# Kernel optimization log

Hardware: AMD Instinct MI355X
Metric: run time of the kernel (lower is better)

## Reference

```python
import jax, jax.numpy as jnp
import numpy as np

NUM_HEADS = 16
THRESHOLD = 4e-4  # < 1/S so every softmax row keeps >=1 entry (classical path of grover_search_filter)


def setup_inputs() -> dict:
    key = jax.random.key(0)
    k0, k1, k2 = jax.random.split(key, 3)
    B, S, E = 4, 1024, 1024
    x = jax.random.normal(k0, (B, S, E), dtype=jnp.float32)
    Wqkv = jax.random.normal(k1, (3 * E, E), dtype=jnp.float32) * 0.02
    bqkv = jnp.zeros((3 * E,), dtype=jnp.float32)
    Wproj = jax.random.normal(k2, (E, E), dtype=jnp.float32) * 0.02
    bproj = jnp.zeros((E,), dtype=jnp.float32)
    return {"x": x, "Wqkv": Wqkv, "bqkv": bqkv, "Wproj": Wproj, "bproj": bproj}


def reference(x, Wqkv, bqkv, Wproj, bproj):
    B, S, E = x.shape
    H = NUM_HEADS
    D = E // H
    scale = D ** -0.5
    # qkv projection -> (3, B, H, S, D), matching torch permute(2,0,3,1,4)
    qkv = (x @ Wqkv.T + bqkv).reshape(B, S, 3, H, D).transpose(2, 0, 3, 1, 4)
    q, k, v = qkv[0], qkv[1], qkv[2]
    attn_logits = jnp.einsum("bhqd,bhkd->bhqk", q, k) * scale  # [B,H,S,S]
    attn_probs = jax.nn.softmax(attn_logits, axis=-1)
    # grover_search_filter: seq_len > 2**max_qubits -> classical threshold mask
    selected = attn_probs > THRESHOLD
    filtered_logits = jnp.where(selected, attn_logits, -jnp.inf)
    filtered_attn = jax.nn.softmax(filtered_logits, axis=-1)
    # dropout is identity in eval mode
    out = jnp.einsum("bhqk,bhkd->bhqd", filtered_attn, v)
    out = out.transpose(0, 2, 1, 3).reshape(B, S, E)
    out = out @ Wproj.T + bproj
    return out, filtered_attn
```

## Files before the change

kernel.cpp:

```cpp
#include <hip/hip_runtime.h>
#include <hip/hip_bf16.h>
#include <cstdint>


#define BB 4
#define SS 1024
#define EE 1024
#define HH 16
#define DD 64

typedef __attribute__((ext_vector_type(8))) short bf16x8;
typedef __attribute__((ext_vector_type(4))) float f32x4;

__global__ __launch_bounds__(256) void split_f32(
    const float* __restrict__ in, __hip_bfloat16* __restrict__ hi,
    __hip_bfloat16* __restrict__ lo, int n4) {
  int i = blockIdx.x * 256 + threadIdx.x;
  if (i >= n4) return;
  float4 v = ((const float4*)in)[i];
  float vv[4] = {v.x, v.y, v.z, v.w};
  __hip_bfloat16 h[4], l[4];
#pragma unroll
  for (int j = 0; j < 4; ++j) {
    h[j] = __float2bfloat16(vv[j]);
    l[j] = __float2bfloat16(vv[j] - __bfloat162float(h[j]));
  }
  ((ushort4*)hi)[i] = *(ushort4*)h;
  if (lo) ((ushort4*)lo)[i] = *(ushort4*)l;
}

template <int MODE>
__global__ __launch_bounds__(256) void gemm(
    const __hip_bfloat16* __restrict__ Ah, const __hip_bfloat16* __restrict__ Al,
    const __hip_bfloat16* __restrict__ Bh, const __hip_bfloat16* __restrict__ Bl,
    const float* __restrict__ Af, const float* __restrict__ bias,
    float* __restrict__ oF, __hip_bfloat16* __restrict__ o1,
    __hip_bfloat16* __restrict__ o2, __hip_bfloat16* __restrict__ o3,
    __hip_bfloat16* __restrict__ o4, __hip_bfloat16* __restrict__ o5,
    int M, int N, int K, int lda, int ldb, long long sA, long long sB) {
  constexpr bool SPLIT = (MODE == 0 || MODE == 1);
  constexpr bool AF32  = (MODE == 2);

  const int tid  = threadIdx.x;
  const int lane = tid & 63;
  const int wave = tid >> 6;
  const int wm   = (wave >> 1) * 64;
  const int wn   = (wave & 1) * 64;
  const int quad = lane >> 4;
  const int l15  = lane & 15;
  const int m0   = blockIdx.y * 128;
  const int n0   = blockIdx.x * 128;
  const long long zz = blockIdx.z;

  if (AF32) Af += zz * sA;
  else { Ah += zz * sA; if (SPLIT) Al += zz * sA; }
  Bh += zz * sB;
  if (SPLIT) Bl += zz * sB;

  __shared__ __align__(16) __hip_bfloat16 lds[(SPLIT ? 4 : 2) * 128 * 72];
  __hip_bfloat16* lAh = lds;
  __hip_bfloat16* lAl = SPLIT ? lds + 128 * 72 : nullptr;
  __hip_bfloat16* lBh = lds + (SPLIT ? 2 : 1) * 128 * 72;
  __hip_bfloat16* lBl = SPLIT ? lds + 3 * 128 * 72 : nullptr;

  f32x4 acc[4][4] = {};

  for (int k0 = 0; k0 < K; k0 += 64) {
#pragma unroll
    for (int it = 0; it < 4; ++it) {
      int flat = (it * 256 + tid) * 8;
      int row  = flat >> 6;
      int kk   = flat & 63;
      const bool mok = (m0 + row < M);
      const bool nok = (n0 + row < N);
      if (AF32) {
        float4 f0 = {0, 0, 0, 0}, f1 = {0, 0, 0, 0};
        if (mok) {
          const float* src = Af + (long long)(m0 + row) * lda + k0 + kk;
          f0 = *(const float4*)src;
          f1 = *(const float4*)(src + 4);
        }
        __hip_bfloat16 t[8];
        t[0] = __float2bfloat16(f0.x); t[1] = __float2bfloat16(f0.y);
        t[2] = __float2bfloat16(f0.z); t[3] = __float2bfloat16(f0.w);
        t[4] = __float2bfloat16(f1.x); t[5] = __float2bfloat16(f1.y);
        t[6] = __float2bfloat16(f1.z); t[7] = __float2bfloat16(f1.w);
        *(uint4*)&lAh[row * 72 + kk] = *(uint4*)t;
      } else {
        uint4 va = {0, 0, 0, 0};
        if (mok) va = *(const uint4*)(Ah + (long long)(m0 + row) * lda + k0 + kk);
        *(uint4*)&lAh[row * 72 + kk] = va;
        if (SPLIT) {
          uint4 vl = {0, 0, 0, 0};
          if (mok) vl = *(const uint4*)(Al + (long long)(m0 + row) * lda + k0 + kk);
          *(uint4*)&lAl[row * 72 + kk] = vl;
        }
      }
      uint4 vb = {0, 0, 0, 0};
      if (nok) vb = *(const uint4*)(Bh + (long long)(n0 + row) * ldb + k0 + kk);
      *(uint4*)&lBh[row * 72 + kk] = vb;
      if (SPLIT) {
        uint4 vbl = {0, 0, 0, 0};
        if (nok) vbl = *(const uint4*)(Bl + (long long)(n0 + row) * ldb + k0 + kk);
        *(uint4*)&lBl[row * 72 + kk] = vbl;
      }
    }
    __syncthreads();

#pragma unroll
    for (int ks = 0; ks < 64; ks += 32) {
      bf16x8 ah[4], bh[4], al[4], bl[4];
#pragma unroll
      for (int i = 0; i < 4; ++i) {
        int off = (wm + i * 16 + l15) * 72 + ks + quad * 8;
        ah[i] = *(const bf16x8*)&lAh[off];
        if (SPLIT) al[i] = *(const bf16x8*)&lAl[off];
      }
#pragma unroll
      for (int j = 0; j < 4; ++j) {
        int off = (wn + j * 16 + l15) * 72 + ks + quad * 8;
        bh[j] = *(const bf16x8*)&lBh[off];
        if (SPLIT) bl[j] = *(const bf16x8*)&lBl[off];
      }
#pragma unroll
      for (int i = 0; i < 4; ++i)
#pragma unroll
        for (int j = 0; j < 4; ++j) {
          if (SPLIT) {
            acc[i][j] = __builtin_amdgcn_mfma_f32_16x16x32_bf16(al[i], bh[j], acc[i][j], 0, 0, 0);
            acc[i][j] = __builtin_amdgcn_mfma_f32_16x16x32_bf16(ah[i], bl[j], acc[i][j], 0, 0, 0);
          }
          acc[i][j] = __builtin_amdgcn_mfma_f32_16x16x32_bf16(ah[i], bh[j], acc[i][j], 0, 0, 0);
        }
    }
    __syncthreads();
  }

#pragma unroll
  for (int i = 0; i < 4; ++i) {
#pragma unroll
    for (int j = 0; j < 4; ++j) {
#pragma unroll
      for (int r = 0; r < 4; ++r) {
        int m = m0 + wm + i * 16 + quad * 4 + r;
        int n = n0 + wn + j * 16 + l15;
        float v = acc[i][j][r];
        if (MODE == 0) {
          v += bias[n];
          int c = n >> 10, nn = n & 1023, h = nn >> 6, d = nn & 63;
          int b = m >> 10, s = m & 1023;
          long long idx = (((long long)(b * HH + h) * SS + s) << 6) + d;
          if (c == 0) {
            __hip_bfloat16 hh = __float2bfloat16(v);
            o1[idx] = hh;
            o2[idx] = __float2bfloat16(v - __bfloat162float(hh));
          } else if (c == 1) {
            __hip_bfloat16 hh = __float2bfloat16(v);
            o3[idx] = hh;
            o4[idx] = __float2bfloat16(v - __bfloat162float(hh));
          } else {
            o5[(((long long)(b * HH + h) * DD + d) << 10) + s] = __float2bfloat16(v);
          }
        } else if (MODE == 1) {
          oF[zz * (SS * SS) + (long long)m * SS + n] = v * 0.125f;
        } else if (MODE == 2) {
          if (n < DD) {
            int b = (int)(zz >> 4), h = (int)(zz & 15);
            o1[(((long long)(b * SS + m)) << 10) + h * DD + n] = __float2bfloat16(v);
          }
        } else {
          oF[(long long)m * EE + n] = v + bias[n];
        }
      }
    }
  }
}

__device__ __forceinline__ float qg_max16(float v) {
#pragma unroll
  for (int o = 8; o > 0; o >>= 1) v = fmaxf(v, __shfl_xor(v, o));
  return v;
}
__device__ __forceinline__ float qg_sum16(float v) {
#pragma unroll
  for (int o = 8; o > 0; o >>= 1) v += __shfl_xor(v, o);
  return v;
}

__global__ __launch_bounds__(256, 4) void fused_attn(
    const __hip_bfloat16* __restrict__ qh, const __hip_bfloat16* __restrict__ ql,
    const __hip_bfloat16* __restrict__ kh, const __hip_bfloat16* __restrict__ kl,
    const __hip_bfloat16* __restrict__ vT, float* __restrict__ attn,
    __hip_bfloat16* __restrict__ ao) {
  const int tid  = threadIdx.x;
  const int lane = tid & 63;
  const int wave = tid >> 6;
  const int quad = lane >> 4;
  const int l15  = lane & 15;

  int id = blockIdx.x;
  const int q8 = gridDim.x >> 3;
  id = (id & 7) * q8 + (id >> 3);
  const int bh = id >> 6;
  const int q0 = (id & 63) * 16;

  const int brow = (bh >> 4) * SS;
  const int h    = bh & 15;
  const long long qbase = ((long long)bh * SS + q0) * DD;
  const long long kbase = (long long)bh * SS * DD;
  const long long vbase = (long long)bh * DD * SS;
  const long long abase = ((long long)bh * SS + q0) * SS;

  __shared__ __align__(16) __hip_bfloat16 Pl[16][1032];
  __shared__ float red[3][4][16];

  bf16x8 aqh0, aqh1, aql0, aql1;
  {
    const __hip_bfloat16* ph = qh + qbase + l15 * DD + quad * 8;
    const __hip_bfloat16* pl = ql + qbase + l15 * DD + quad * 8;
    aqh0 = *(const bf16x8*)(ph);
    aqh1 = *(const bf16x8*)(ph + 32);
    aql0 = *(const bf16x8*)(pl);
    aql1 = *(const bf16x8*)(pl + 32);
  }

  f32x4 acc[16];
  const __hip_bfloat16* pkh0 = kh + kbase + (long long)(wave * 256 + l15) * DD + quad * 8;
  const __hip_bfloat16* pkl0 = kl + kbase + (long long)(wave * 256 + l15) * DD + quad * 8;
#pragma unroll
  for (int nt = 0; nt < 16; ++nt) {
    const __hip_bfloat16* pkh = pkh0 + nt * 16 * DD;
    const __hip_bfloat16* pkl = pkl0 + nt * 16 * DD;
    bf16x8 b0 = *(const bf16x8*)(pkh);
    bf16x8 b1 = *(const bf16x8*)(pkh + 32);
    bf16x8 c0 = *(const bf16x8*)(pkl);
    bf16x8 c1 = *(const bf16x8*)(pkl + 32);
    f32x4 a = {};
    a = __builtin_amdgcn_mfma_f32_16x16x32_bf16(aql0, b0, a, 0, 0, 0);
    a = __builtin_amdgcn_mfma_f32_16x16x32_bf16(aqh0, c0, a, 0, 0, 0);
    a = __builtin_amdgcn_mfma_f32_16x16x32_bf16(aqh0, b0, a, 0, 0, 0);
    a = __builtin_amdgcn_mfma_f32_16x16x32_bf16(aql1, b1, a, 0, 0, 0);
    a = __builtin_amdgcn_mfma_f32_16x16x32_bf16(aqh1, c1, a, 0, 0, 0);
    a = __builtin_amdgcn_mfma_f32_16x16x32_bf16(aqh1, b1, a, 0, 0, 0);
    acc[nt] = a;
  }

#pragma unroll
  for (int nt = 0; nt < 16; ++nt)
#pragma unroll
    for (int r = 0; r < 4; ++r) acc[nt][r] *= 0.125f;

  float mx[4];
#pragma unroll
  for (int r = 0; r < 4; ++r) {
    float mm = acc[0][r];
#pragma unroll
    for (int nt = 1; nt < 16; ++nt) mm = fmaxf(mm, acc[nt][r]);
    mx[r] = qg_max16(mm);
  }
  if (l15 == 0) {
#pragma unroll
    for (int r = 0; r < 4; ++r) red[0][wave][quad * 4 + r] = mx[r];
  }
  __syncthreads();
  float m[4];
#pragma unroll
  for (int r = 0; r < 4; ++r) {
    const int q = quad * 4 + r;
    m[r] = fmaxf(fmaxf(red[0][0][q], red[0][1][q]),
                 fmaxf(red[0][2][q], red[0][3][q]));
  }

  float zl[4] = {0.f, 0.f, 0.f, 0.f};
#pragma unroll
  for (int nt = 0; nt < 16; ++nt)
#pragma unroll
    for (int r = 0; r < 4; ++r) {
      float e = expf(acc[nt][r] - m[r]);
      acc[nt][r] = e;
      zl[r] += e;
    }
#pragma unroll
  for (int r = 0; r < 4; ++r) zl[r] = qg_sum16(zl[r]);
  if (l15 == 0) {
#pragma unroll
    for (int r = 0; r < 4; ++r) red[1][wave][quad * 4 + r] = zl[r];
  }
  __syncthreads();
  float c[4];
#pragma unroll
  for (int r = 0; r < 4; ++r) {
    const int q = quad * 4 + r;
    const float Z = (red[1][0][q] + red[1][1][q]) + (red[1][2][q] + red[1][3][q]);
    c[r] = 4e-4f * Z;
  }

  float sl[4] = {0.f, 0.f, 0.f, 0.f};
#pragma unroll
  for (int nt = 0; nt < 16; ++nt)
#pragma unroll
    for (int r = 0; r < 4; ++r)
      if (acc[nt][r] > c[r]) sl[r] += acc[nt][r];
#pragma unroll
  for (int r = 0; r < 4; ++r) sl[r] = qg_sum16(sl[r]);
  if (l15 == 0) {
#pragma unroll
    for (int r = 0; r < 4; ++r) red[2][wave][quad * 4 + r] = sl[r];
  }
  __syncthreads();
  float rinv[4];
#pragma unroll
  for (int r = 0; r < 4; ++r) {
    const int q = quad * 4 + r;
    const float Zs = (red[2][0][q] + red[2][1][q]) + (red[2][2][q] + red[2][3][q]);
    rinv[r] = 1.0f / Zs;
  }

#pragma unroll
  for (int nt = 0; nt < 16; ++nt) {
    const int k = wave * 256 + nt * 16 + l15;
#pragma unroll
    for (int r = 0; r < 4; ++r) {
      const int q = quad * 4 + r;
      const float e = acc[nt][r];
      const float p = (e > c[r]) ? e * rinv[r] : 0.f;
      attn[abase + (long long)q * SS + k] = p;
      Pl[q][k] = __float2bfloat16(p);
    }
  }
  __syncthreads();

  const int d0 = wave * 16;
  f32x4 o0 = {}, o1 = {};
  const __hip_bfloat16* pv = vT + vbase + (long long)(d0 + l15) * SS + quad * 8;
  const __hip_bfloat16* pp = &Pl[l15][0] + quad * 8;
#pragma unroll
  for (int ks = 0; ks < 32; ks += 2) {
    bf16x8 a0 = *(const bf16x8*)(pp + ks * 32);
    bf16x8 v0 = *(const bf16x8*)(pv + ks * 32);
    o0 = __builtin_amdgcn_mfma_f32_16x16x32_bf16(a0, v0, o0, 0, 0, 0);
    bf16x8 a1 = *(const bf16x8*)(pp + (ks + 1) * 32);
    bf16x8 v1 = *(const bf16x8*)(pv + (ks + 1) * 32);
    o1 = __builtin_amdgcn_mfma_f32_16x16x32_bf16(a1, v1, o1, 0, 0, 0);
  }
#pragma unroll
  for (int r = 0; r < 4; ++r) {
    const int q = q0 + quad * 4 + r;
    ao[((long long)(brow + q)) * EE + h * DD + d0 + l15] =
        __float2bfloat16(o0[r] + o1[r]);
  }
}

extern "C" void kernel_launch(void* const* d_in, const int* in_sizes, int n_in,
                              void* d_out, int out_size, void* d_ws, size_t ws_size,
                              hipStream_t stream) {
  const float* x     = (const float*)d_in[0];
  const float* Wqkv  = (const float*)d_in[1];
  const float* bqkv  = (const float*)d_in[2];
  const float* Wproj = (const float*)d_in[3];
  const float* bproj = (const float*)d_in[4];

  float* out   = (float*)d_out;
  float* attnF = out + (size_t)BB * SS * EE;

  const size_t M1 = 1024 * 1024;
  __hip_bfloat16* w = (__hip_bfloat16*)d_ws;

  if (ws_size >= (size_t)80 * 1024 * 1024) {
    __hip_bfloat16 *xh = w, *xl = xh + 4 * M1;
    __hip_bfloat16 *Wqh = xl + 4 * M1, *Wql = Wqh + 3 * M1, *Wph = Wql + 3 * M1;
    __hip_bfloat16 *qh = Wph + M1, *ql = qh + 4 * M1, *kh = ql + 4 * M1, *kl = kh + 4 * M1;
    __hip_bfloat16 *vT = kl + 4 * M1, *ao = vT + 4 * M1;

    split_f32<<<4096, 256, 0, stream>>>(x, xh, xl, 1024 * 1024);
    split_f32<<<3072, 256, 0, stream>>>(Wqkv, Wqh, Wql, 768 * 1024);
    split_f32<<<1024, 256, 0, stream>>>(Wproj, Wph, nullptr, 256 * 1024);

    gemm<0><<<dim3(24, 32, 1), 256, 0, stream>>>(
        xh, xl, Wqh, Wql, nullptr, bqkv, nullptr, qh, ql, kh, kl, vT,
        4096, 3072, 1024, 1024, 1024, 0LL, 0LL);
    fused_attn<<<dim3(BB * HH * 64), 256, 0, stream>>>(
        qh, ql, kh, kl, vT, attnF, ao);
    gemm<3><<<dim3(8, 32, 1), 256, 0, stream>>>(
        ao, nullptr, Wph, nullptr, nullptr, bproj, out, nullptr, nullptr, nullptr, nullptr, nullptr,
        4096, 1024, 1024, 1024, 1024, 0LL, 0LL);
    return;
  }

  __hip_bfloat16 *Wqh = w, *Wql = Wqh + 3 * M1, *Wph = Wql + 3 * M1;
  __hip_bfloat16 *xh = Wph + M1, *xl = xh + M1;
  __hip_bfloat16 *qh = xl + M1, *ql = qh + M1, *kh = ql + M1, *kl = kh + M1;
  __hip_bfloat16 *vT = kl + M1, *ao = vT + M1;

  split_f32<<<3072, 256, 0, stream>>>(Wqkv, Wqh, Wql, 768 * 1024);
  split_f32<<<1024, 256, 0, stream>>>(Wproj, Wph, nullptr, 256 * 1024);

  for (int b = 0; b < BB; ++b) {
    const float* xb   = x + (size_t)b * SS * EE;
    float* attnb      = attnF + (size_t)b * HH * SS * SS;
    float* outb       = out + (size_t)b * SS * EE;

    split_f32<<<1024, 256, 0, stream>>>(xb, xh, xl, 256 * 1024);
    gemm<0><<<dim3(24, 8, 1), 256, 0, stream>>>(
        xh, xl, Wqh, Wql, nullptr, bqkv, nullptr, qh, ql, kh, kl, vT,
        1024, 3072, 1024, 1024, 1024, 0LL, 0LL);
    fused_attn<<<dim3(HH * 64), 256, 0, stream>>>(
        qh, ql, kh, kl, vT, attnb, ao);
    gemm<3><<<dim3(8, 8, 1), 256, 0, stream>>>(
        ao, nullptr, Wph, nullptr, nullptr, bproj, outb, nullptr, nullptr, nullptr, nullptr, nullptr,
        1024, 1024, 1024, 1024, 1024, 0LL, 0LL);
  }
}
```

Before: 691.5 us.

## Split fused attention across eight waves with split-K PV reduction

The attention block grows from 256 to 512 threads. Each wave now handles 128 keys instead of 256, and the P·V product is split over two key halves that are reduced through a small shared buffer. The change also adds s_setprio around MFMA groups and nontemporal stores for the large attention-probability output. The goal is lower per-wave register pressure and more latency hiding. The cost is an extra barrier, more cross-wave reductions, and possibly lower occupancy because the larger shared allocation has to fit 512-thread blocks.

```diff
diff --git a/kernel.cpp b/kernel.cpp
--- a/kernel.cpp
+++ b/kernel.cpp
@@ -187,7 +187,7 @@
   return v;
 }
 
-__global__ __launch_bounds__(256, 4) void fused_attn(
+__global__ __launch_bounds__(512, 6) void fused_attn(
     const __hip_bfloat16* __restrict__ qh, const __hip_bfloat16* __restrict__ ql,
     const __hip_bfloat16* __restrict__ kh, const __hip_bfloat16* __restrict__ kl,
     const __hip_bfloat16* __restrict__ vT, float* __restrict__ attn,
@@ -212,7 +212,8 @@
   const long long abase = ((long long)bh * SS + q0) * SS;
 
   __shared__ __align__(16) __hip_bfloat16 Pl[16][1032];
-  __shared__ float red[3][4][16];
+  __shared__ float red[3][8][16];
+  __shared__ float Obuf[4][16][18];
 
   bf16x8 aqh0, aqh1, aql0, aql1;
   {
@@ -224,11 +225,11 @@
     aql1 = *(const bf16x8*)(pl + 32);
   }
 
-  f32x4 acc[16];
-  const __hip_bfloat16* pkh0 = kh + kbase + (long long)(wave * 256 + l15) * DD + quad * 8;
-  const __hip_bfloat16* pkl0 = kl + kbase + (long long)(wave * 256 + l15) * DD + quad * 8;
-#pragma unroll
-  for (int nt = 0; nt < 16; ++nt) {
+  f32x4 acc[8];
+  const __hip_bfloat16* pkh0 = kh + kbase + (long long)(wave * 128 + l15) * DD + quad * 8;
+  const __hip_bfloat16* pkl0 = kl + kbase + (long long)(wave * 128 + l15) * DD + quad * 8;
+#pragma unroll
+  for (int nt = 0; nt < 8; ++nt) {
     const __hip_bfloat16* pkh = pkh0 + nt * 16 * DD;
     const __hip_bfloat16* pkl = pkl0 + nt * 16 * DD;
     bf16x8 b0 = *(const bf16x8*)(pkh);
@@ -236,17 +237,19 @@
     bf16x8 c0 = *(const bf16x8*)(pkl);
     bf16x8 c1 = *(const bf16x8*)(pkl + 32);
     f32x4 a = {};
+    __builtin_amdgcn_s_setprio(1);
     a = __builtin_amdgcn_mfma_f32_16x16x32_bf16(aql0, b0, a, 0, 0, 0);
     a = __builtin_amdgcn_mfma_f32_16x16x32_bf16(aqh0, c0, a, 0, 0, 0);
     a = __builtin_amdgcn_mfma_f32_16x16x32_bf16(aqh0, b0, a, 0, 0, 0);
     a = __builtin_amdgcn_mfma_f32_16x16x32_bf16(aql1, b1, a, 0, 0, 0);
     a = __builtin_amdgcn_mfma_f32_16x16x32_bf16(aqh1, c1, a, 0, 0, 0);
     a = __builtin_amdgcn_mfma_f32_16x16x32_bf16(aqh1, b1, a, 0, 0, 0);
+    __builtin_amdgcn_s_setprio(0);
     acc[nt] = a;
   }
 
 #pragma unroll
-  for (int nt = 0; nt < 16; ++nt)
+  for (int nt = 0; nt < 8; ++nt)
 #pragma unroll
     for (int r = 0; r < 4; ++r) acc[nt][r] *= 0.125f;
 
@@ -255,7 +258,7 @@
   for (int r = 0; r < 4; ++r) {
     float mm = acc[0][r];
 #pragma unroll
-    for (int nt = 1; nt < 16; ++nt) mm = fmaxf(mm, acc[nt][r]);
+    for (int nt = 1; nt < 8; ++nt) mm = fmaxf(mm, acc[nt][r]);
     mx[r] = qg_max16(mm);
   }
   if (l15 == 0) {
@@ -267,13 +270,16 @@
 #pragma unroll
   for (int r = 0; r < 4; ++r) {
     const int q = quad * 4 + r;
-    m[r] = fmaxf(fmaxf(red[0][0][q], red[0][1][q]),
-                 fmaxf(red[0][2][q], red[0][3][q]));
+    float a01 = fmaxf(red[0][0][q], red[0][1][q]);
+    float a23 = fmaxf(red[0][2][q], red[0][3][q]);
+    float a45 = fmaxf(red[0][4][q], red[0][5][q]);
+    float a67 = fmaxf(red[0][6][q], red[0][7][q]);
+    m[r] = fmaxf(fmaxf(a01, a23), fmaxf(a45, a67));
   }
 
   float zl[4] = {0.f, 0.f, 0.f, 0.f};
 #pragma unroll
-  for (int nt = 0; nt < 16; ++nt)
+  for (int nt = 0; nt < 8; ++nt)
 #pragma unroll
     for (int r = 0; r < 4; ++r) {
       float e = expf(acc[nt][r] - m[r]);
@@ -291,13 +297,14 @@
 #pragma unroll
   for (int r = 0; r < 4; ++r) {
     const int q = quad * 4 + r;
-    const float Z = (red[1][0][q] + red[1][1][q]) + (red[1][2][q] + red[1][3][q]);
+    const float Z = ((red[1][0][q] + red[1][1][q]) + (red[1][2][q] + red[1][3][q])) +
+                    ((red[1][4][q] + red[1][5][q]) + (red[1][6][q] + red[1][7][q]));
     c[r] = 4e-4f * Z;
   }
 
   float sl[4] = {0.f, 0.f, 0.f, 0.f};
 #pragma unroll
-  for (int nt = 0; nt < 16; ++nt)
+  for (int nt = 0; nt < 8; ++nt)
 #pragma unroll
     for (int r = 0; r < 4; ++r)
       if (acc[nt][r] > c[r]) sl[r] += acc[nt][r];
@@ -312,42 +319,54 @@
 #pragma unroll
   for (int r = 0; r < 4; ++r) {
     const int q = quad * 4 + r;
-    const float Zs = (red[2][0][q] + red[2][1][q]) + (red[2][2][q] + red[2][3][q]);
+    const float Zs = ((red[2][0][q] + red[2][1][q]) + (red[2][2][q] + red[2][3][q])) +
+                     ((red[2][4][q] + red[2][5][q]) + (red[2][6][q] + red[2][7][q]));
     rinv[r] = 1.0f / Zs;
   }
 
 #pragma unroll
-  for (int nt = 0; nt < 16; ++nt) {
-    const int k = wave * 256 + nt * 16 + l15;
+  for (int nt = 0; nt < 8; ++nt) {
+    const int k = wave * 128 + nt * 16 + l15;
 #pragma unroll
     for (int r = 0; r < 4; ++r) {
       const int q = quad * 4 + r;
       const float e = acc[nt][r];
       const float p = (e > c[r]) ? e * rinv[r] : 0.f;
-      attn[abase + (long long)q * SS + k] = p;
+      __builtin_nontemporal_store(p, &attn[abase + (long long)q * SS + k]);
       Pl[q][k] = __float2bfloat16(p);
     }
   }
   __syncthreads();
 
-  const int d0 = wave * 16;
+  const int d0  = (wave & 3) * 16;
+  const int kh2 = (wave >> 2) * 512;
   f32x4 o0 = {}, o1 = {};
-  const __hip_bfloat16* pv = vT + vbase + (long long)(d0 + l15) * SS + quad * 8;
-  const __hip_bfloat16* pp = &Pl[l15][0] + quad * 8;
-#pragma unroll
-  for (int ks = 0; ks < 32; ks += 2) {
+  const __hip_bfloat16* pv = vT + vbase + (long long)(d0 + l15) * SS + kh2 + quad * 8;
+  const __hip_bfloat16* pp = &Pl[l15][kh2] + quad * 8;
+#pragma unroll
+  for (int ks = 0; ks < 16; ks += 2) {
     bf16x8 a0 = *(const bf16x8*)(pp + ks * 32);
     bf16x8 v0 = *(const bf16x8*)(pv + ks * 32);
-    o0 = __builtin_amdgcn_mfma_f32_16x16x32_bf16(a0, v0, o0, 0, 0, 0);
     bf16x8 a1 = *(const bf16x8*)(pp + (ks + 1) * 32);
     bf16x8 v1 = *(const bf16x8*)(pv + (ks + 1) * 32);
+    __builtin_amdgcn_s_setprio(1);
+    o0 = __builtin_amdgcn_mfma_f32_16x16x32_bf16(a0, v0, o0, 0, 0, 0);
     o1 = __builtin_amdgcn_mfma_f32_16x16x32_bf16(a1, v1, o1, 0, 0, 0);
-  }
-#pragma unroll
-  for (int r = 0; r < 4; ++r) {
-    const int q = q0 + quad * 4 + r;
-    ao[((long long)(brow + q)) * EE + h * DD + d0 + l15] =
-        __float2bfloat16(o0[r] + o1[r]);
+    __builtin_amdgcn_s_setprio(0);
+  }
+  if (wave >= 4) {
+#pragma unroll
+    for (int r = 0; r < 4; ++r)
+      Obuf[wave & 3][quad * 4 + r][l15] = o0[r] + o1[r];
+  }
+  __syncthreads();
+  if (wave < 4) {
+#pragma unroll
+    for (int r = 0; r < 4; ++r) {
+      const int q = q0 + quad * 4 + r;
+      const float v = o0[r] + o1[r] + Obuf[wave][quad * 4 + r][l15];
+      ao[((long long)(brow + q)) * EE + h * DD + d0 + l15] = __float2bfloat16(v);
+    }
   }
 }
 
@@ -379,7 +398,7 @@
     gemm<0><<<dim3(24, 32, 1), 256, 0, stream>>>(
         xh, xl, Wqh, Wql, nullptr, bqkv, nullptr, qh, ql, kh, kl, vT,
         4096, 3072, 1024, 1024, 1024, 0LL, 0LL);
-    fused_attn<<<dim3(BB * HH * 64), 256, 0, stream>>>(
+    fused_attn<<<dim3(BB * HH * 64), 512, 0, stream>>>(
         qh, ql, kh, kl, vT, attnF, ao);
     gemm<3><<<dim3(8, 32, 1), 256, 0, stream>>>(
         ao, nullptr, Wph, nullptr, nullptr, bproj, out, nullptr, nullptr, nullptr, nullptr, nullptr,
@@ -404,7 +423,7 @@
     gemm<0><<<dim3(24, 8, 1), 256, 0, stream>>>(
         xh, xl, Wqh, Wql, nullptr, bqkv, nullptr, qh, ql, kh, kl, vT,
         1024, 3072, 1024, 1024, 1024, 0LL, 0LL);
-    fused_attn<<<dim3(HH * 64), 256, 0, stream>>>(
+    fused_attn<<<dim3(HH * 64), 512, 0, stream>>>(
         qh, ql, kh, kl, vT, attnb, ao);
     gemm<3><<<dim3(8, 8, 1), 256, 0, stream>>>(
         ao, nullptr, Wph, nullptr, nullptr, bproj, outb, nullptr, nullptr, nullptr, nullptr, nullptr,
```

New measurement: 668.9 us. 3.3% less time.
